# Performance work log

Hardware: AMD Instinct MI355X
Metric: run time of the kernel (lower is better)

## Reference

```python
import jax, jax.numpy as jnp
import numpy as np
jax.config.update("jax_enable_x64", True)

PRIMES = [2654435761, 2246822519, 3266489917, 2028178513, 1220703125, 1610612741, 805306457, 402653189, 3674653429, 2860486313, 1073676287, 2971215073, 1500450271, 3267000013, 2654435789, 4049292737]
WINDOWS = [1, 2, 4, 8]
BUCKETS = 2000000
SIGN_BITS = 8
BOUNDARY = 2
OFFSETS = (1, 2, 3, 4, 5, 6, 7, 8)
CHUNK = 32


def layer_norm(x, w, b, eps=1e-5):
    m = jnp.mean(x, axis=-1, keepdims=True)
    v = jnp.var(x, axis=-1, keepdims=True)
    return (x - m) * jax.lax.rsqrt(v + eps) * w + b


def shift_right(tokens, off):
    T = tokens.shape[1]
    return jnp.pad(tokens, ((0, 0), (off, 0)))[:, :T]


def hash_scale(tokens, window):
    # rolling polynomial hash: XOR of prime-multiplied shifted tokens
    h = jnp.zeros_like(tokens)
    for i in range(window):
        off = i + 1
        if off >= tokens.shape[1]:
            continue
        h = h ^ (shift_right(tokens, off) * PRIMES[i % len(PRIMES)])
    return h % BUCKETS


def tiny_scan(x, gw, gb, iw, ib, ow, ob, lnw, lnb):
    # chunked cumsum-based linear recurrence h_t = a_t * h_{t-1} + (1-a_t) * u_t
    B, T, D = x.shape
    S = gw.shape[0]
    K = min(CHUNK, T)
    g = jax.nn.sigmoid(jnp.einsum('btd,sd->bts', x, gw) + gb)
    drive = (1.0 - g) * (jnp.einsum('btd,sd->bts', x, iw) + ib)
    nC = T // K  # T chosen divisible by CHUNK
    a = g.reshape(B, nC, K, S)
    b = drive.reshape(B, nC, K, S)
    log_a = jnp.log(jnp.maximum(a, 1e-6))
    cum_a = jnp.exp(jnp.cumsum(log_a, axis=2))             # [B,nC,K,S]
    inv_cum_a = 1.0 / jnp.maximum(cum_a, 1e-8)
    cum_wb = jnp.cumsum(b * inv_cum_a, axis=2)

    def step(h, cs):
        ca, cw = cs                                        # [B,K,S]
        out = ca * (h[:, None, :] + cw)
        return out[:, -1], out

    h0 = jnp.zeros((B, S), x.dtype)
    _, outs = jax.lax.scan(step, h0, (jnp.swapaxes(cum_a, 0, 1), jnp.swapaxes(cum_wb, 0, 1)))
    states = jnp.swapaxes(outs, 0, 1).reshape(B, T, S)
    y = jnp.einsum('bts,ds->btd', states, ow) + ob
    return layer_norm(x + y, lnw, lnb)


def forward(chars, byte_embed, table0, table1, table2, table3, cond_w, conv_w, conv_b,
            gate_w, gate_b, inpr_w, inpr_b, outpr_w, outpr_b, scan_ln_w, scan_ln_b,
            inp_w, inp_b, r_w1, r_w2, r_proj, r_ln_w, r_ln_b, out_w, out_b):
    tokens = chars.astype(jnp.int64)
    B, T = tokens.shape
    tables = [table0, table1, table2, table3]
    keys = [hash_scale(tokens, WINDOWS[s]) for s in range(4)]
    short = [tables[s][keys[s]] for s in range(BOUNDARY)]     # each [B,T,2]
    # condition long-scale keys on sign bits of short-scale features
    cond_logits = jnp.einsum('btd,sd->bts', jnp.concatenate(short, axis=-1), cond_w)
    bits = (cond_logits > 0).astype(jnp.int64)                # [B,T,8]
    cond_key = jnp.zeros((B, T), dtype=jnp.int64)
    for i in range(SIGN_BITS):
        cond_key = cond_key ^ (bits[..., i] * PRIMES[i])
    longe = [tables[s][(keys[s] ^ cond_key) % BUCKETS] for s in range(BOUNDARY, 4)]
    hash_feat = jnp.concatenate(short + longe, axis=-1)       # [B,T,8]
    # causal depthwise conv over hash features
    C = hash_feat.shape[-1]
    ht = jnp.swapaxes(hash_feat, 1, 2)                        # [B,C,T]
    Kc = conv_w.shape[-1]
    conv = jax.lax.conv_general_dilated(ht, conv_w, (1,), [(Kc - 1, 0)],
                                        dimension_numbers=('NCH', 'OIH', 'NCH'),
                                        feature_group_count=C)
    hash_feat = jax.nn.silu(jnp.swapaxes(conv + conv_b[None, :, None], 1, 2))
    byte_emb = byte_embed[tokens]                             # [B,T,64]
    # match features: equality with k-shifted sequence
    mfs = []
    for k in OFFSETS:
        m = (tokens == shift_right(tokens, k)).astype(jnp.float32)
        m = m.at[:, :k].set(0.0)
        mfs.append(m)
    mf = jnp.stack(mfs, axis=-1)                              # [B,T,8]
    h = jnp.concatenate([byte_emb, hash_feat, mf], axis=-1)   # [B,T,80]
    h = tiny_scan(h, gate_w, gate_b, inpr_w, inpr_b, outpr_w, outpr_b, scan_ln_w, scan_ln_b)
    h = jax.nn.silu(jnp.einsum('btd,hd->bth', h, inp_w) + inp_b)   # [B,T,256]
    hh = jnp.einsum('bth,dh->btd',
                    jax.nn.silu(jnp.einsum('btd,hd->bth', h, r_w1)) * jnp.einsum('btd,hd->bth', h, r_w2),
                    r_proj)
    h = layer_norm(hh + h, r_ln_w, r_ln_b)
    return jnp.einsum('bth,vh->btv', h, out_w) + out_b        # [B,T,1024]


def setup_inputs() -> dict:
    key = jax.random.key(0)
    ks = jax.random.split(key, 32)
    f32 = jnp.float32
    B, T, V, EB, S, D, H = 32, 2048, 1024, 64, 32, 80, 256

    def rn(k, shape, std):
        return jax.random.normal(k, shape, dtype=f32) * std

    return {
        'chars': jax.random.randint(ks[0], (B, T), 0, V, dtype=jnp.int64),
        'byte_embed': rn(ks[1], (V, EB), 0.02),
        'table0': rn(ks[2], (BUCKETS, 2), 0.02),
        'table1': rn(ks[3], (BUCKETS, 2), 0.02),
        'table2': rn(ks[4], (BUCKETS, 2), 0.02),
        'table3': rn(ks[5], (BUCKETS, 2), 0.02),
        'cond_w': rn(ks[6], (SIGN_BITS, 2 * BOUNDARY), 0.3),
        'conv_w': rn(ks[7], (8, 1, 8), 0.2),
        'conv_b': rn(ks[8], (8,), 0.02),
        'gate_w': rn(ks[9], (S, D), 0.1),
        'gate_b': rn(ks[10], (S,), 0.02),
        'inpr_w': rn(ks[11], (S, D), 0.1),
        'inpr_b': rn(ks[12], (S,), 0.02),
        'outpr_w': rn(ks[13], (D, S), 0.1),
        'outpr_b': rn(ks[14], (D,), 0.02),
        'scan_ln_w': jnp.ones((D,), f32),
        'scan_ln_b': jnp.zeros((D,), f32),
        'inp_w': rn(ks[15], (H, D), 0.1),
        'inp_b': rn(ks[16], (H,), 0.02),
        'r_w1': rn(ks[17], (H, H), 0.05),
        'r_w2': rn(ks[18], (H, H), 0.05),
        'r_proj': rn(ks[19], (H, H), 0.05),
        'r_ln_w': jnp.ones((H,), f32),
        'r_ln_b': jnp.zeros((H,), f32),
        'out_w': rn(ks[20], (V, H), 0.05),
        'out_b': rn(ks[21], (V,), 0.02),
    }


def reference(chars, byte_embed, table0, table1, table2, table3, cond_w, conv_w, conv_b,
              gate_w, gate_b, inpr_w, inpr_b, outpr_w, outpr_b, scan_ln_w, scan_ln_b,
              inp_w, inp_b, r_w1, r_w2, r_proj, r_ln_w, r_ln_b, out_w, out_b):
    return forward(chars, byte_embed, table0, table1, table2, table3, cond_w, conv_w, conv_b,
                   gate_w, gate_b, inpr_w, inpr_b, outpr_w, outpr_b, scan_ln_w, scan_ln_b,
                   inp_w, inp_b, r_w1, r_w2, r_proj, r_ln_w, r_ln_b, out_w, out_b)
```

## Files before the change

### kernel.cpp

```cpp
#include <hip/hip_runtime.h>

#define BB 32
#define TT 2048
#define SS 32
#define DD 80
#define HH 256
#define VV 1024
#define EBD 64

typedef unsigned short u16;
typedef __attribute__((ext_vector_type(8))) __bf16 bf16x8;
typedef __attribute__((ext_vector_type(4))) float f32x4;

#define MFMA(a, b, c) __builtin_amdgcn_mfma_f32_16x16x32_bf16(a, b, c, 0, 0, 0)

__device__ inline u16 f2bu(float f) {
    unsigned u = __float_as_uint(f);
    return (u16)((u + 0x7FFFu + ((u >> 16) & 1u)) >> 16);
}
__device__ inline __bf16 f2b(float f) {
    u16 r = f2bu(f);
    return __builtin_bit_cast(__bf16, r);
}
__device__ inline float b2f(u16 h) { return __uint_as_float(((unsigned)h) << 16); }

__device__ inline bf16x8 ldfrag(const u16* base, int row, int k0, int lane) {
    return *(const bf16x8*)(base + (size_t)row * 256 + k0 + ((lane >> 4) << 3));
}
__device__ inline bf16x8 ldfrag96(const u16* base, int row, int k0, int lane) {
    return *(const bf16x8*)(base + (size_t)row * 96 + k0 + ((lane >> 4) << 3));
}

__global__ __launch_bounds__(256) void k_prep(const float* __restrict__ w1,
                                              const float* __restrict__ w2,
                                              const float* __restrict__ wp,
                                              const float* __restrict__ ow,
                                              const float* __restrict__ iw,
                                              u16* __restrict__ wbf) {
    int i = blockIdx.x * 256 + threadIdx.x;
    if (i >= 483328) return;
    float v;
    if (i < 65536) v = w1[i];
    else if (i < 131072) v = w2[i - 65536];
    else if (i < 196608) v = wp[i - 131072];
    else if (i < 458752) v = ow[i - 196608];
    else {
        int j = i - 458752;
        int row = j / 96, col = j % 96;
        v = (col < 80) ? iw[row * 80 + col] : 0.f;
    }
    wbf[i] = f2bu(v);
}

__global__ __launch_bounds__(256) void k_hash(const int* __restrict__ tok,
                                              const float* __restrict__ t0,
                                              const float* __restrict__ t1,
                                              const float* __restrict__ t2,
                                              const float* __restrict__ t3,
                                              const float* __restrict__ cond_w,
                                              float* __restrict__ raw) {
    int idx = blockIdx.x * 256 + threadIdx.x;
    if (idx >= BB * TT) return;
    int b = idx / TT, t = idx % TT;
    const int* tr = tok + b * TT;

    unsigned long long tv[8];
#pragma unroll
    for (int i = 0; i < 8; i++) {
        int ts = t - 1 - i;
        tv[i] = (ts >= 0) ? (unsigned long long)(unsigned)tr[ts] : 0ull;
    }
    const unsigned long long P[8] = {2654435761ull, 2246822519ull, 3266489917ull,
                                     2028178513ull, 1220703125ull, 1610612741ull,
                                     805306457ull, 402653189ull};
    unsigned long long x = 0ull;
    x ^= tv[0] * P[0]; unsigned long long k0 = x % 2000000ull;
    x ^= tv[1] * P[1]; unsigned long long k1 = x % 2000000ull;
    x ^= tv[2] * P[2]; x ^= tv[3] * P[3]; unsigned long long k2 = x % 2000000ull;
    x ^= tv[4] * P[4]; x ^= tv[5] * P[5];
    x ^= tv[6] * P[6]; x ^= tv[7] * P[7]; unsigned long long k3 = x % 2000000ull;

    float f0 = t0[k0 * 2], f1 = t0[k0 * 2 + 1];
    float f2 = t1[k1 * 2], f3 = t1[k1 * 2 + 1];

    unsigned long long ck = 0ull;
#pragma unroll
    for (int j = 0; j < 8; j++) {
        float lg = f0 * cond_w[j * 4 + 0] + f1 * cond_w[j * 4 + 1] +
                   f2 * cond_w[j * 4 + 2] + f3 * cond_w[j * 4 + 3];
        if (lg > 0.f) ck ^= P[j];
    }
    unsigned long long lk2 = (k2 ^ ck) % 2000000ull;
    unsigned long long lk3 = (k3 ^ ck) % 2000000ull;

    float* o = raw + (size_t)idx * 8;
    o[0] = f0; o[1] = f1; o[2] = f2; o[3] = f3;
    o[4] = t2[lk2 * 2]; o[5] = t2[lk2 * 2 + 1];
    o[6] = t3[lk3 * 2]; o[7] = t3[lk3 * 2 + 1];
}

__global__ __launch_bounds__(256) void k_featgates(const int* __restrict__ tok,
                                                   const float* __restrict__ be,
                                                   const float* __restrict__ raw,
                                                   const float* __restrict__ conv_w,
                                                   const float* __restrict__ conv_b,
                                                   const float* __restrict__ gw,
                                                   const float* __restrict__ gb,
                                                   const float* __restrict__ iw,
                                                   const float* __restrict__ ib,
                                                   float* __restrict__ hf,
                                                   float* __restrict__ Ag,
                                                   float* __restrict__ Dr) {
    __shared__ float xs[64][DD];
    __shared__ float gws[32 * 81];
    __shared__ float iws[32 * 81];
    int blk = blockIdx.x;
    int b = blk >> 5;
    int t0 = (blk & 31) << 6;
    int tid = threadIdx.x;
    const int* tr = tok + b * TT;

    for (int i = tid; i < 32 * 80; i += 256) {
        int s = i / 80, d = i % 80;
        gws[s * 81 + d] = gw[i];
        iws[s * 81 + d] = iw[i];
    }

    for (int i = tid; i < 1024; i += 256) {
        int row = i >> 4, q = i & 15;
        int t = t0 + row;
        int tk = tr[t];
        f32x4 v = *(const f32x4*)(be + (size_t)tk * EBD + q * 4);
        *(f32x4*)&xs[row][q * 4] = v;
        *(f32x4*)(hf + ((size_t)(b * TT + t)) * DD + q * 4) = v;
    }

    if (tid < 64) {
        int t = t0 + tid;
        int tk = tr[t];
        float* o = hf + ((size_t)(b * TT + t)) * DD;
#pragma unroll
        for (int c = 0; c < 8; c++) {
            float acc = conv_b[c];
#pragma unroll
            for (int k = 0; k < 8; k++) {
                int ts = t - 7 + k;
                if (ts >= 0) acc += conv_w[c * 8 + k] * raw[((size_t)(b * TT + ts)) * 8 + c];
            }
            float sv = acc / (1.f + expf(-acc));
            xs[tid][64 + c] = sv;
            o[64 + c] = sv;
        }
#pragma unroll
        for (int k = 1; k <= 8; k++) {
            float m = (t >= k && tk == tr[t - k]) ? 1.f : 0.f;
            xs[tid][71 + k] = m;
            o[71 + k] = m;
        }
    }
    __syncthreads();

    for (int p = tid; p < 64 * SS; p += 256) {
        int s = p & 31, tt = p >> 5;
        float ga = gb[s], ia = ib[s];
        for (int d = 0; d < DD; d++) {
            float xv = xs[tt][d];
            ga += xv * gws[s * 81 + d];
            ia += xv * iws[s * 81 + d];
        }
        float g = 1.f / (1.f + expf(-ga));
        float drv = (1.f - g) * ia;
        size_t oo = ((size_t)(b * SS + s)) * TT + t0 + tt;
        Ag[oo] = g;
        Dr[oo] = drv;
    }
}

__global__ __launch_bounds__(64) void k_scan_par(const float* __restrict__ Ag,
                                                 const float* __restrict__ Dr,
                                                 float* __restrict__ st) {
    int bs = blockIdx.x;
    int b = bs >> 5, s = bs & 31;
    int c = threadIdx.x;
    const float* ar = Ag + (size_t)bs * TT + c * 32;
    const float* dr = Dr + (size_t)bs * TT + c * 32;

    float ca[32], cw[32];
    float lacc = 0.f, wacc = 0.f;
#pragma unroll
    for (int k = 0; k < 32; k += 4) {
        f32x4 av = *(const f32x4*)(ar + k);
        f32x4 dv = *(const f32x4*)(dr + k);
#pragma unroll
        for (int j = 0; j < 4; j++) {
            lacc += logf(fmaxf(av[j], 1e-6f));
            float cav = expf(lacc);
            ca[k + j] = cav;
            wacc += dv[j] / fmaxf(cav, 1e-8f);
            cw[k + j] = wacc;
        }
    }

    float A = ca[31];
    float Bc = ca[31] * wacc;
    for (int off = 1; off < 64; off <<= 1) {
        float Ap = __shfl_up(A, off, 64);
        float Bp = __shfl_up(Bc, off, 64);
        if (c >= off) {
            Bc = A * Bp + Bc;
            A = A * Ap;
        }
    }
    float h0 = __shfl_up(Bc, 1, 64);
    if (c == 0) h0 = 0.f;

    float* op = st + ((size_t)(b * TT + c * 32)) * SS + s;
#pragma unroll
    for (int k = 0; k < 32; k++)
        op[(size_t)k * SS] = ca[k] * (h0 + cw[k]);
}

__global__ __launch_bounds__(256) void k_post(const float* __restrict__ st,
                                              const float* __restrict__ hf,
                                              const float* __restrict__ ow,
                                              const float* __restrict__ ob,
                                              const float* __restrict__ lnw,
                                              const float* __restrict__ lnb,
                                              u16* __restrict__ h1p) {
    __shared__ float ows[DD * SS];
    for (int i = threadIdx.x; i < DD * SS; i += 256) ows[i] = ow[i];
    __syncthreads();

    int idx = blockIdx.x * 256 + threadIdx.x;
    if (idx >= BB * TT) return;
    const float* sp = st + (size_t)idx * SS;
    float sv[SS];
#pragma unroll
    for (int i = 0; i < SS; i += 4) {
        f32x4 v4 = *(const f32x4*)(sp + i);
        sv[i] = v4[0]; sv[i + 1] = v4[1]; sv[i + 2] = v4[2]; sv[i + 3] = v4[3];
    }
    const float* x = hf + (size_t)idx * DD;

    float s1 = 0.f, s2 = 0.f;
    for (int d = 0; d < DD; d++) {
        float acc = ob[d];
#pragma unroll
        for (int i = 0; i < SS; i++) acc += sv[i] * ows[d * SS + i];
        float v = acc + x[d];
        s1 += v; s2 += v * v;
    }
    float m = s1 * (1.f / DD);
    float var = s2 * (1.f / DD) - m * m;
    float rs = rsqrtf(var + 1e-5f);
    u16* o = h1p + (size_t)idx * 96;
    for (int d = 0; d < DD; d++) {
        float acc = ob[d];
#pragma unroll
        for (int i = 0; i < SS; i++) acc += sv[i] * ows[d * SS + i];
        float v = acc + x[d];
        o[d] = f2bu((v - m) * rs * lnw[d] + lnb[d]);
    }
    *(f32x4*)(o + 80) = f32x4{0.f, 0.f, 0.f, 0.f};
    *(f32x4*)(o + 88) = f32x4{0.f, 0.f, 0.f, 0.f};
}

#define SX 264
__global__ __launch_bounds__(256) void k_gmlp_f(const u16* __restrict__ h1p,
                                                const u16* __restrict__ iwb,
                                                const float* __restrict__ ibias,
                                                const u16* __restrict__ w1,
                                                const u16* __restrict__ w2,
                                                const u16* __restrict__ wp,
                                                const float* __restrict__ lnw,
                                                const float* __restrict__ lnb,
                                                u16* __restrict__ h3) {
    __shared__ u16 Xs[64 * SX];
    __shared__ u16 Us[64 * SX];
    __shared__ float redS[64][4], redQ[64][4];
    int lane = threadIdx.x & 63, wv = threadIdx.x >> 6;
    int r0 = blockIdx.x * 64;
    int g = lane >> 4, cl = lane & 15, rl = lane & 15;

    {
        int c0 = wv * 64;
        f32x4 acc[4][4] = {};
#pragma unroll
        for (int ks = 0; ks < 3; ks++) {
            int k0 = ks * 32;
            bf16x8 a[4];
#pragma unroll
            for (int mi = 0; mi < 4; mi++) a[mi] = ldfrag96(h1p, r0 + mi * 16 + rl, k0, lane);
#pragma unroll
            for (int ni = 0; ni < 4; ni++) {
                bf16x8 b = ldfrag96(iwb, c0 + ni * 16 + rl, k0, lane);
#pragma unroll
                for (int mi = 0; mi < 4; mi++) acc[mi][ni] = MFMA(a[mi], b, acc[mi][ni]);
            }
        }
#pragma unroll
        for (int ni = 0; ni < 4; ni++) {
            float bv = ibias[c0 + ni * 16 + cl];
#pragma unroll
            for (int mi = 0; mi < 4; mi++)
#pragma unroll
                for (int r = 0; r < 4; r++) {
                    float v = acc[mi][ni][r] + bv;
                    Xs[(mi * 16 + g * 4 + r) * SX + c0 + ni * 16 + cl] =
                        f2bu(v / (1.f + expf(-v)));
                }
        }
    }
    __syncthreads();

    for (int cg = 0; cg < 2; cg++) {
        int c0 = cg * 128 + wv * 32;
        f32x4 a1[4][2] = {}, a2[4][2] = {};
        for (int ks = 0; ks < 8; ks++) {
            int k0 = ks * 32 + (g << 3);
            bf16x8 a[4];
#pragma unroll
            for (int mi = 0; mi < 4; mi++)
                a[mi] = *(const bf16x8*)&Xs[(mi * 16 + rl) * SX + k0];
#pragma unroll
            for (int ni = 0; ni < 2; ni++) {
                bf16x8 b1 = ldfrag(w1, c0 + ni * 16 + rl, ks * 32, lane);
                bf16x8 b2 = ldfrag(w2, c0 + ni * 16 + rl, ks * 32, lane);
#pragma unroll
                for (int mi = 0; mi < 4; mi++) {
                    a1[mi][ni] = MFMA(a[mi], b1, a1[mi][ni]);
                    a2[mi][ni] = MFMA(a[mi], b2, a2[mi][ni]);
                }
            }
        }
#pragma unroll
        for (int mi = 0; mi < 4; mi++)
#pragma unroll
            for (int ni = 0; ni < 2; ni++)
#pragma unroll
                for (int r = 0; r < 4; r++) {
                    float v1 = a1[mi][ni][r], v2 = a2[mi][ni][r];
                    float u = v1 / (1.f + expf(-v1)) * v2;
                    Us[(mi * 16 + g * 4 + r) * SX + c0 + ni * 16 + cl] = f2bu(u);
                }
    }
    __syncthreads();

    {
        int c0 = wv * 64;
        f32x4 acc[4][4] = {};
        for (int ks = 0; ks < 8; ks++) {
            int k0 = ks * 32 + (g << 3);
            bf16x8 a[4];
#pragma unroll
            for (int mi = 0; mi < 4; mi++)
                a[mi] = *(const bf16x8*)&Us[(mi * 16 + rl) * SX + k0];
#pragma unroll
            for (int ni = 0; ni < 4; ni++) {
                bf16x8 b = ldfrag(wp, c0 + ni * 16 + rl, ks * 32, lane);
#pragma unroll
                for (int mi = 0; mi < 4; mi++) acc[mi][ni] = MFMA(a[mi], b, acc[mi][ni]);
            }
        }
#pragma unroll
        for (int mi = 0; mi < 4; mi++)
#pragma unroll
            for (int r = 0; r < 4; r++) {
                float s = 0.f, q = 0.f;
                int row = mi * 16 + g * 4 + r;
#pragma unroll
                for (int ni = 0; ni < 4; ni++) {
                    int col = c0 + ni * 16 + cl;
                    float v = acc[mi][ni][r] + b2f(Xs[row * SX + col]);
                    acc[mi][ni][r] = v;
                    s += v; q += v * v;
                }
                for (int m = 1; m < 16; m <<= 1) {
                    s += __shfl_xor(s, m, 64);
                    q += __shfl_xor(q, m, 64);
                }
                if (cl == 0) { redS[row][wv] = s; redQ[row][wv] = q; }
            }
        __syncthreads();

        float lw[4], lb[4];
#pragma unroll
        for (int ni = 0; ni < 4; ni++) {
            lw[ni] = lnw[c0 + ni * 16 + cl];
            lb[ni] = lnb[c0 + ni * 16 + cl];
        }
#pragma unroll
        for (int mi = 0; mi < 4; mi++)
#pragma unroll
            for (int r = 0; r < 4; r++) {
                int row = mi * 16 + g * 4 + r;
                float S = redS[row][0] + redS[row][1] + redS[row][2] + redS[row][3];
                float Q = redQ[row][0] + redQ[row][1] + redQ[row][2] + redQ[row][3];
                float m = S * (1.f / 256.f);
                float rs = rsqrtf(Q * (1.f / 256.f) - m * m + 1e-5f);
#pragma unroll
                for (int ni = 0; ni < 4; ni++) {
                    float y = (acc[mi][ni][r] - m) * rs * lw[ni] + lb[ni];
                    h3[(size_t)(r0 + row) * 256 + c0 + ni * 16 + cl] = f2bu(y);
                }
            }
    }
}

#define SA 40
__global__ __launch_bounds__(256) void k_out4(const u16* __restrict__ h3,
                                              const u16* __restrict__ ow,
                                              const float* __restrict__ bias,
                                              float* __restrict__ out) {
    __shared__ u16 As[2][128 * SA];
    __shared__ u16 Bs[2][128 * SA];
    int tid = threadIdx.x, lane = tid & 63, wv = tid >> 6;
    int r0 = blockIdx.x * 128;
    int wr = (wv >> 1) * 64, wc = (wv & 1) * 64;
    int rl = lane & 15, g = lane >> 4;

    int row0_ = tid >> 2, cc0_ = tid & 3;
    int row1_ = (tid + 256) >> 2, cc1_ = tid & 3;
    bf16x8 rA0, rA1, rB0, rB1;

#define LOADT(cg, kt)                                                                      \
    {                                                                                      \
        int kbase = (kt) * 32;                                                             \
        int c0g = (cg) * 128;                                                              \
        rA0 = *(const bf16x8*)(h3 + (size_t)(r0 + row0_) * 256 + kbase + cc0_ * 8);        \
        rA1 = *(const bf16x8*)(h3 + (size_t)(r0 + row1_) * 256 + kbase + cc1_ * 8);        \
        rB0 = *(const bf16x8*)(ow + (size_t)(c0g + row0_) * 256 + kbase + cc0_ * 8);       \
        rB1 = *(const bf16x8*)(ow + (size_t)(c0g + row1_) * 256 + kbase + cc1_ * 8);       \
    }
#define WRITET(buf)                                                                        \
    {                                                                                      \
        *(bf16x8*)&As[buf][row0_ * SA + cc0_ * 8] = rA0;                                   \
        *(bf16x8*)&As[buf][row1_ * SA + cc1_ * 8] = rA1;                                   \
        *(bf16x8*)&Bs[buf][row0_ * SA + cc0_ * 8] = rB0;                                   \
        *(bf16x8*)&Bs[buf][row1_ * SA + cc1_ * 8] = rB1;                                   \
    }

    for (int cg = 0; cg < 8; cg++) {
        LOADT(cg, 0);
        WRITET(0);
        f32x4 acc[4][4] = {};
        for (int kt = 0; kt < 8; kt++) {
            int buf = kt & 1;
            if (kt < 7) LOADT(cg, kt + 1);
            __syncthreads();
            bf16x8 a[4], b[4];
#pragma unroll
            for (int mi = 0; mi < 4; mi++)
                a[mi] = *(const bf16x8*)&As[buf][(wr + mi * 16 + rl) * SA + g * 8];
#pragma unroll
            for (int ni = 0; ni < 4; ni++)
                b[ni] = *(const bf16x8*)&Bs[buf][(wc + ni * 16 + rl) * SA + g * 8];
#pragma unroll
            for (int ni = 0; ni < 4; ni++)
#pragma unroll
                for (int mi = 0; mi < 4; mi++) acc[mi][ni] = MFMA(a[mi], b[ni], acc[mi][ni]);
            if (kt < 7) WRITET(buf ^ 1);
        }
        int c0g = cg * 128;
        int cl = lane & 15;
#pragma unroll
        for (int ni = 0; ni < 4; ni++) {
            float bv = bias[c0g + wc + ni * 16 + cl];
#pragma unroll
            for (int mi = 0; mi < 4; mi++)
#pragma unroll
                for (int r = 0; r < 4; r++)
                    out[(size_t)(r0 + wr + mi * 16 + g * 4 + r) * VV + c0g + wc + ni * 16 + cl] =
                        acc[mi][ni][r] + bv;
        }
        __syncthreads();
    }
#undef LOADT
#undef WRITET
}

extern "C" void kernel_launch(void* const* d_in, const int* in_sizes, int n_in,
                              void* d_out, int out_size, void* d_ws, size_t ws_size,
                              hipStream_t stream) {
    const int* chars        = (const int*)d_in[0];
    const float* byte_embed = (const float*)d_in[1];
    const float* table0     = (const float*)d_in[2];
    const float* table1     = (const float*)d_in[3];
    const float* table2     = (const float*)d_in[4];
    const float* table3     = (const float*)d_in[5];
    const float* cond_w     = (const float*)d_in[6];
    const float* conv_w     = (const float*)d_in[7];
    const float* conv_b     = (const float*)d_in[8];
    const float* gate_w     = (const float*)d_in[9];
    const float* gate_b     = (const float*)d_in[10];
    const float* inpr_w     = (const float*)d_in[11];
    const float* inpr_b     = (const float*)d_in[12];
    const float* outpr_w    = (const float*)d_in[13];
    const float* outpr_b    = (const float*)d_in[14];
    const float* scan_ln_w  = (const float*)d_in[15];
    const float* scan_ln_b  = (const float*)d_in[16];
    const float* inp_w      = (const float*)d_in[17];
    const float* inp_b      = (const float*)d_in[18];
    const float* r_w1       = (const float*)d_in[19];
    const float* r_w2       = (const float*)d_in[20];
    const float* r_proj     = (const float*)d_in[21];
    const float* r_ln_w     = (const float*)d_in[22];
    const float* r_ln_b     = (const float*)d_in[23];
    const float* out_w      = (const float*)d_in[24];
    const float* out_b      = (const float*)d_in[25];

    char* ws = (char*)d_ws;
    u16*   wbf = (u16*)(ws + 0);
    u16*   w1b = wbf;
    u16*   w2b = wbf + 65536;
    u16*   wpb = wbf + 131072;
    u16*   owb = wbf + 196608;
    u16*   iwb = wbf + 458752;
    float* hf  = (float*)(ws + 1048576);
    float* raw = (float*)(ws + 23068672);
    float* Ag  = (float*)(ws + 25165824);
    float* Dr  = (float*)(ws + 33554432);
    float* st  = (float*)(ws + 41943040);
    u16*   h1p = (u16*)(ws + 50331648);
    u16*   h3b = (u16*)(ws + 1048576);
    float* out = (float*)d_out;

    k_prep <<<1888, 256, 0, stream>>>(r_w1, r_w2, r_proj, out_w, inp_w, wbf);
    k_hash <<<256, 256, 0, stream>>>(chars, table0, table1, table2, table3, cond_w, raw);
    k_featgates<<<1024, 256, 0, stream>>>(chars, byte_embed, raw, conv_w, conv_b,
                                          gate_w, gate_b, inpr_w, inpr_b, hf, Ag, Dr);
    k_scan_par<<<1024, 64, 0, stream>>>(Ag, Dr, st);
    k_post <<<256, 256, 0, stream>>>(st, hf, outpr_w, outpr_b, scan_ln_w, scan_ln_b, h1p);
    k_gmlp_f<<<1024, 256, 0, stream>>>(h1p, iwb, inp_b, w1b, w2b, wpb, r_ln_w, r_ln_b, h3b);
    k_out4 <<<512, 256, 0, stream>>>(h3b, owb, out_b, out);
}
```

Measured before the change: 336.6 us.

## Halve gMLP kernel LDS by reusing X buffer and holding residual in registers

The fused gMLP kernel drops its second 64x264 shared buffer. The SiLU residual is kept packed in registers, the gated intermediate is staged in registers and then written back into the X buffer after a barrier. The middle GEMM loop is restructured to produce one 16-column slice at a time to limit accumulator registers. A launch bound of 3 blocks per CU is requested. Together these aim for higher occupancy, at the cost of extra register pressure, an extra barrier, and less ILP in the middle GEMM.

```diff
diff --git a/kernel.cpp b/kernel.cpp
--- a/kernel.cpp
+++ b/kernel.cpp
@@ -266,22 +266,23 @@
 }
 
 #define SX 264
-__global__ __launch_bounds__(256) void k_gmlp_f(const u16* __restrict__ h1p,
-                                                const u16* __restrict__ iwb,
-                                                const float* __restrict__ ibias,
-                                                const u16* __restrict__ w1,
-                                                const u16* __restrict__ w2,
-                                                const u16* __restrict__ wp,
-                                                const float* __restrict__ lnw,
-                                                const float* __restrict__ lnb,
-                                                u16* __restrict__ h3) {
+__global__ __launch_bounds__(256, 3) void k_gmlp_f2(const u16* __restrict__ h1p,
+                                                    const u16* __restrict__ iwb,
+                                                    const float* __restrict__ ibias,
+                                                    const u16* __restrict__ w1,
+                                                    const u16* __restrict__ w2,
+                                                    const u16* __restrict__ wp,
+                                                    const float* __restrict__ lnw,
+                                                    const float* __restrict__ lnb,
+                                                    u16* __restrict__ h3) {
     __shared__ u16 Xs[64 * SX];
-    __shared__ u16 Us[64 * SX];
     __shared__ float redS[64][4], redQ[64][4];
     int lane = threadIdx.x & 63, wv = threadIdx.x >> 6;
     int r0 = blockIdx.x * 64;
     int g = lane >> 4, cl = lane & 15, rl = lane & 15;
 
+    unsigned xres[4][4][2];
+
     {
         int c0 = wv * 64;
         f32x4 acc[4][4] = {};
@@ -306,44 +307,60 @@
 #pragma unroll
                 for (int r = 0; r < 4; r++) {
                     float v = acc[mi][ni][r] + bv;
-                    Xs[(mi * 16 + g * 4 + r) * SX + c0 + ni * 16 + cl] =
-                        f2bu(v / (1.f + expf(-v)));
+                    u16 h = f2bu(v / (1.f + expf(-v)));
+                    Xs[(mi * 16 + g * 4 + r) * SX + c0 + ni * 16 + cl] = h;
+                    if (r & 1) xres[mi][ni][r >> 1] |= ((unsigned)h) << 16;
+                    else       xres[mi][ni][r >> 1] = h;
                 }
         }
     }
     __syncthreads();
 
+    unsigned ureg[2][2][4][2];
+#pragma unroll
     for (int cg = 0; cg < 2; cg++) {
-        int c0 = cg * 128 + wv * 32;
-        f32x4 a1[4][2] = {}, a2[4][2] = {};
-        for (int ks = 0; ks < 8; ks++) {
-            int k0 = ks * 32 + (g << 3);
-            bf16x8 a[4];
+#pragma unroll
+        for (int nio = 0; nio < 2; nio++) {
+            int c0 = cg * 128 + wv * 32 + nio * 16;
+            f32x4 a1a[4] = {}, a2a[4] = {};
+            for (int ks = 0; ks < 8; ks++) {
+                int k0 = ks * 32 + (g << 3);
+                bf16x8 a[4];
+#pragma unroll
+                for (int mi = 0; mi < 4; mi++)
+                    a[mi] = *(const bf16x8*)&Xs[(mi * 16 + rl) * SX + k0];
+                bf16x8 b1 = ldfrag(w1, c0 + rl, ks * 32, lane);
+                bf16x8 b2 = ldfrag(w2, c0 + rl, ks * 32, lane);
+#pragma unroll
+                for (int mi = 0; mi < 4; mi++) {
+                    a1a[mi] = MFMA(a[mi], b1, a1a[mi]);
+                    a2a[mi] = MFMA(a[mi], b2, a2a[mi]);
+                }
+            }
 #pragma unroll
             for (int mi = 0; mi < 4; mi++)
-                a[mi] = *(const bf16x8*)&Xs[(mi * 16 + rl) * SX + k0];
-#pragma unroll
-            for (int ni = 0; ni < 2; ni++) {
-                bf16x8 b1 = ldfrag(w1, c0 + ni * 16 + rl, ks * 32, lane);
-                bf16x8 b2 = ldfrag(w2, c0 + ni * 16 + rl, ks * 32, lane);
-#pragma unroll
-                for (int mi = 0; mi < 4; mi++) {
-                    a1[mi][ni] = MFMA(a[mi], b1, a1[mi][ni]);
-                    a2[mi][ni] = MFMA(a[mi], b2, a2[mi][ni]);
-                }
-            }
-        }
-#pragma unroll
-        for (int mi = 0; mi < 4; mi++)
-#pragma unroll
-            for (int ni = 0; ni < 2; ni++)
 #pragma unroll
                 for (int r = 0; r < 4; r++) {
-                    float v1 = a1[mi][ni][r], v2 = a2[mi][ni][r];
-                    float u = v1 / (1.f + expf(-v1)) * v2;
-                    Us[(mi * 16 + g * 4 + r) * SX + c0 + ni * 16 + cl] = f2bu(u);
-                }
-    }
+                    float v1 = a1a[mi][r], v2 = a2a[mi][r];
+                    u16 h = f2bu(v1 / (1.f + expf(-v1)) * v2);
+                    if (r & 1) ureg[cg][nio][mi][r >> 1] |= ((unsigned)h) << 16;
+                    else       ureg[cg][nio][mi][r >> 1] = h;
+                }
+        }
+    }
+    __syncthreads();
+
+#pragma unroll
+    for (int cg = 0; cg < 2; cg++)
+#pragma unroll
+        for (int nio = 0; nio < 2; nio++)
+#pragma unroll
+            for (int mi = 0; mi < 4; mi++)
+#pragma unroll
+                for (int r = 0; r < 4; r++) {
+                    u16 h = (u16)(ureg[cg][nio][mi][r >> 1] >> ((r & 1) * 16));
+                    Xs[(mi * 16 + g * 4 + r) * SX + cg * 128 + wv * 32 + nio * 16 + cl] = h;
+                }
     __syncthreads();
 
     {
@@ -354,7 +371,7 @@
             bf16x8 a[4];
 #pragma unroll
             for (int mi = 0; mi < 4; mi++)
-                a[mi] = *(const bf16x8*)&Us[(mi * 16 + rl) * SX + k0];
+                a[mi] = *(const bf16x8*)&Xs[(mi * 16 + rl) * SX + k0];
 #pragma unroll
             for (int ni = 0; ni < 4; ni++) {
                 bf16x8 b = ldfrag(wp, c0 + ni * 16 + rl, ks * 32, lane);
@@ -370,8 +387,8 @@
                 int row = mi * 16 + g * 4 + r;
 #pragma unroll
                 for (int ni = 0; ni < 4; ni++) {
-                    int col = c0 + ni * 16 + cl;
-                    float v = acc[mi][ni][r] + b2f(Xs[row * SX + col]);
+                    u16 hx = (u16)(xres[mi][ni][r >> 1] >> ((r & 1) * 16));
+                    float v = acc[mi][ni][r] + b2f(hx);
                     acc[mi][ni][r] = v;
                     s += v; q += v * v;
                 }
@@ -531,6 +548,6 @@
                                           gate_w, gate_b, inpr_w, inpr_b, hf, Ag, Dr);
     k_scan_par<<<1024, 64, 0, stream>>>(Ag, Dr, st);
     k_post <<<256, 256, 0, stream>>>(st, hf, outpr_w, outpr_b, scan_ln_w, scan_ln_b, h1p);
-    k_gmlp_f<<<1024, 256, 0, stream>>>(h1p, iwb, inp_b, w1b, w2b, wpb, r_ln_w, r_ln_b, h3b);
+    k_gmlp_f2<<<1024, 256, 0, stream>>>(h1p, iwb, inp_b, w1b, w2b, wpb, r_ln_w, r_ln_b, h3b);
     k_out4 <<<512, 256, 0, stream>>>(h3b, owb, out_b, out);
 }
```

Measured after the change: 412.7 us. 1.23x slower.
